# Performance work log

Hardware: AMD Instinct MI355X
Metric: run time of the kernel (lower is better)

Reference implementation:

```python
import jax, jax.numpy as jnp
import numpy as np

N_HEAD = 16


def setup_inputs() -> dict:
    key = jax.random.key(0)
    ks = jax.random.split(key, 6)
    B, T, C = 8, 1024, 1024
    s = 0.02
    return {
        "x": jax.random.normal(ks[0], (B, T, C), dtype=jnp.float32),
        "Wk": jax.random.normal(ks[1], (C, C), dtype=jnp.float32) * s,
        "bk": jnp.zeros((C,), dtype=jnp.float32),
        "Wq": jax.random.normal(ks[2], (C, C), dtype=jnp.float32) * s,
        "bq": jnp.zeros((C,), dtype=jnp.float32),
        "Wv": jax.random.normal(ks[3], (C, C), dtype=jnp.float32) * s,
        "bv": jnp.zeros((C,), dtype=jnp.float32),
        "Wp": jax.random.normal(ks[4], (C, C), dtype=jnp.float32) * s,
        "bp": jnp.zeros((C,), dtype=jnp.float32),
    }


def reference(x, Wk, bk, Wq, bq, Wv, bv, Wp, bp):
    B, T, C = x.shape
    H = N_HEAD
    d = C // H
    # QKV projections, split heads -> [B, H, T, d]
    k = (x @ Wk + bk).reshape(B, T, H, d).transpose(0, 2, 1, 3)
    q = (x @ Wq + bq).reshape(B, T, H, d).transpose(0, 2, 1, 3)
    v = (x @ Wv + bv).reshape(B, T, H, d).transpose(0, 2, 1, 3)
    # NOTE: original computes K @ Q^T (not Q @ K^T) and scales by C^-0.5
    attn = jnp.einsum('bhid,bhjd->bhij', k, q) * (C ** -0.5)
    mask = jnp.tril(jnp.ones((T, T), dtype=bool))  # tril==0 positions masked
    attn = jnp.where(mask, attn, -jnp.inf)
    attn = jax.nn.softmax(attn, axis=-1)
    out = jnp.einsum('bhij,bhjd->bhid', attn, v)  # [B, H, T, d]
    out = out.transpose(0, 2, 1, 3).reshape(B, T, C)
    return out @ Wp + bp
```

## Files before the change

### kernel.cpp

```cpp
#include <hip/hip_runtime.h>

typedef unsigned short u16;
typedef unsigned int u32;
typedef __bf16 bf16x8 __attribute__((ext_vector_type(8)));
typedef float f32x4 __attribute__((ext_vector_type(4)));

__device__ __forceinline__ u16 f2bf(float f) {
  u32 u = __builtin_bit_cast(u32, f);
  u += 0x7fffu + ((u >> 16) & 1u);
  return (u16)(u >> 16);
}

#define GLOAD_LDS16(g, l) __builtin_amdgcn_global_load_lds( \
    (const __attribute__((address_space(1))) void*)(g),     \
    (__attribute__((address_space(3))) void*)(l), 16, 0, 0)

#define SCK (0.03125f * 1.44269504088896f)

__global__ __launch_bounds__(256) void cvt_x_k(const float* __restrict__ x,
                                               u16* __restrict__ xb) {
  size_t i = (size_t)blockIdx.x * 256 + threadIdx.x;
  const float4* p = reinterpret_cast<const float4*>(x) + i * 2;
  float4 a = p[0], b = p[1];
  u32 w0 = f2bf(a.x) | ((u32)f2bf(a.y) << 16);
  u32 w1 = f2bf(a.z) | ((u32)f2bf(a.w) << 16);
  u32 w2 = f2bf(b.x) | ((u32)f2bf(b.y) << 16);
  u32 w3 = f2bf(b.z) | ((u32)f2bf(b.w) << 16);
  uint4 o; o.x = w0; o.y = w1; o.z = w2; o.w = w3;
  *reinterpret_cast<uint4*>(xb + i * 8) = o;
}

__global__ __launch_bounds__(256) void transW_k(const float* __restrict__ W0,
                                                const float* __restrict__ W1,
                                                const float* __restrict__ W2,
                                                const float* __restrict__ W3,
                                                u16* __restrict__ WT) {
  __shared__ float tile[64][65];
  const float* W = blockIdx.z == 0 ? W0 : blockIdx.z == 1 ? W1
                 : blockIdx.z == 2 ? W2 : W3;
  u16* dst = WT + (size_t)blockIdx.z * 1024 * 1024;
  const int k0 = blockIdx.x * 64, n0 = blockIdx.y * 64;
  const int tid = threadIdx.x;
  const int rr = tid >> 4, c4 = (tid & 15) * 4;
#pragma unroll
  for (int p = 0; p < 4; ++p) {
    int r = rr + p * 16;
    float4 v = *reinterpret_cast<const float4*>(W + (size_t)(k0 + r) * 1024 + n0 + c4);
    tile[r][c4 + 0] = v.x; tile[r][c4 + 1] = v.y;
    tile[r][c4 + 2] = v.z; tile[r][c4 + 3] = v.w;
  }
  __syncthreads();
#pragma unroll
  for (int p = 0; p < 4; ++p) {
    int nl = rr + p * 16;
    u32 w0 = f2bf(tile[c4 + 0][nl]) | ((u32)f2bf(tile[c4 + 1][nl]) << 16);
    u32 w1 = f2bf(tile[c4 + 2][nl]) | ((u32)f2bf(tile[c4 + 3][nl]) << 16);
    uint2 o; o.x = w0; o.y = w1;
    *reinterpret_cast<uint2*>(dst + (size_t)(n0 + nl) * 1024 + k0 + c4) = o;
  }
}

template <int MODE>
__global__ __launch_bounds__(256) void gemm_k(
    const u16* __restrict__ A, const u16* __restrict__ BT,
    const float* __restrict__ bias0, const float* __restrict__ bias1,
    const float* __restrict__ bias2,
    u16* __restrict__ out_k, u16* __restrict__ out_q, u16* __restrict__ out_vT,
    float* __restrict__ out_f) {
  __shared__ __align__(16) u16 As[128 * 32];
  __shared__ __align__(16) u16 Bs[128 * 32];
  const int tid = threadIdx.x;
  const int row0 = blockIdx.x * 128, col0 = blockIdx.y * 128;
  const int w = tid >> 6, lane = tid & 63;
  const int wr = (w >> 1) * 64, wc = (w & 1) * 64;
  const int fr = lane & 15, fq = lane >> 4, koff = fq * 8;

  const int e0 = tid * 8;
  const int srow = e0 >> 5, scol = e0 & 31;
  const u16* Ag = A + (size_t)(row0 + srow) * 1024 + scol;
  const u16* Bg = BT + (size_t)(col0 + srow) * 1024 + scol;

  f32x4 acc[4][4] = {};

  for (int kt = 0; kt < 32; ++kt) {
    const int k0 = kt * 32;
    GLOAD_LDS16(Ag + k0, &As[e0]);
    GLOAD_LDS16(Ag + k0 + 64 * 1024, &As[e0 + 2048]);
    GLOAD_LDS16(Bg + k0, &Bs[e0]);
    GLOAD_LDS16(Bg + k0 + 64 * 1024, &Bs[e0 + 2048]);
    __syncthreads();
    bf16x8 a[4], b[4];
#pragma unroll
    for (int m = 0; m < 4; ++m)
      a[m] = *reinterpret_cast<const bf16x8*>(&As[(wr + m * 16 + fr) * 32 + koff]);
#pragma unroll
    for (int n = 0; n < 4; ++n)
      b[n] = *reinterpret_cast<const bf16x8*>(&Bs[(wc + n * 16 + fr) * 32 + koff]);
#pragma unroll
    for (int m = 0; m < 4; ++m)
#pragma unroll
      for (int n = 0; n < 4; ++n)
        acc[m][n] = __builtin_amdgcn_mfma_f32_16x16x32_bf16(a[m], b[n], acc[m][n], 0, 0, 0);
    __syncthreads();
  }

  if constexpr (MODE == 0) {
    const int which = col0 >> 10;
    const float* bias = which == 0 ? bias0 : which == 1 ? bias1 : bias2;
#pragma unroll
    for (int m = 0; m < 4; ++m) {
#pragma unroll
      for (int n = 0; n < 4; ++n) {
        const int rg = row0 + wr + m * 16 + fq * 4;
        const int cg = col0 + wc + n * 16 + fr;
        const int nloc = cg & 1023;
        const float bv = bias[nloc];
        if (which == 0) {
#pragma unroll
          for (int r = 0; r < 4; ++r)
            out_k[(size_t)(rg + r) * 1024 + nloc] = f2bf((acc[m][n][r] + bv) * SCK);
        } else if (which == 1) {
#pragma unroll
          for (int r = 0; r < 4; ++r)
            out_q[(size_t)(rg + r) * 1024 + nloc] = f2bf(acc[m][n][r] + bv);
        } else {
          const int bb = rg >> 10, t = rg & 1023;
          const int h = nloc >> 6, dl = nloc & 63;
          u32 w0 = f2bf(acc[m][n][0] + bv) | ((u32)f2bf(acc[m][n][1] + bv) << 16);
          u32 w1 = f2bf(acc[m][n][2] + bv) | ((u32)f2bf(acc[m][n][3] + bv) << 16);
          uint2 ov; ov.x = w0; ov.y = w1;
          *reinterpret_cast<uint2*>(out_vT + ((size_t)(bb * 16 + h) * 64 + dl) * 1024 + t) = ov;
        }
      }
    }
  } else {
#pragma unroll
    for (int m = 0; m < 4; ++m)
#pragma unroll
      for (int n = 0; n < 4; ++n) {
        const int rg = row0 + wr + m * 16 + fq * 4;
        const int cg = col0 + wc + n * 16 + fr;
        const float bv = bias0[cg];
#pragma unroll
        for (int r = 0; r < 4; ++r)
          out_f[(size_t)(rg + r) * 1024 + cg] = acc[m][n][r] + bv;
      }
  }
}

__global__ __launch_bounds__(256, 4) void attn_k(const u16* __restrict__ Q,
                                                 const u16* __restrict__ K,
                                                 const u16* __restrict__ vT,
                                                 u16* __restrict__ O) {
  __shared__ __align__(16) u16 KsA[4096], KsB[4096], VsA[4096], VsB[4096];
  __shared__ __align__(16) u16 Plds[4][16][40];
  const int tid = threadIdx.x;
  const int w = tid >> 6, lane = tid & 63;
  const int fr = lane & 15, fq = lane >> 4, koff = fq * 8;

  const int n = blockIdx.x + 8 * (blockIdx.y + 16 * blockIdx.z);
  const int xcd = n & 7, rest = n >> 3;
  const int g = rest >> 3, pair = rest & 7;
  const int hb = xcd + 8 * g;
  const int h = hb & 15, b = hb >> 4;

  const size_t bstride = (size_t)1024 * 1024;
  const u16* Qb = Q + b * bstride + h * 64;
  const u16* Kg = K + b * bstride + h * 64;
  const u16* Vg = vT + ((size_t)(b * 16 + h) * 64) * 1024;

  const int srow = tid >> 3;
  const int scb = (tid & 7) ^ (srow & 7);
  const u16* KgT = Kg + (size_t)srow * 1024 + scb * 8;
  const u16* VgT = Vg + (size_t)srow * 1024 + scb * 8;

  const int vK0 = fr * 128 + ((fq ^ (fr & 7)) << 4);
  const int vK1 = vK0 ^ 64;
  const int pw = w * 1280 + fq * 320 + fr * 2;
  const int pr = w * 1280 + fr * 80 + fq * 16;

#define STAGE(KS, VS, jt) do {                                          \
    GLOAD_LDS16(KgT + (size_t)(jt) * 65536, &KS[tid * 8]);              \
    GLOAD_LDS16(KgT + (size_t)(jt) * 65536 + 32 * 1024, &KS[2048 + tid * 8]); \
    GLOAD_LDS16(VgT + (jt) * 64, &VS[tid * 8]);                         \
    GLOAD_LDS16(VgT + (jt) * 64 + 32 * 1024, &VS[2048 + tid * 8]);      \
  } while (0)

#pragma unroll 1
  for (int ph = 0; ph < 2; ++ph) {
    const int T = ph ? (15 - pair) : pair;
    const int i0 = T * 64;
    const int ibase = i0 + w * 16;

    bf16x8 aq0 = *reinterpret_cast<const bf16x8*>(&Qb[(size_t)(ibase + fr) * 1024 + koff]);
    bf16x8 aq1 = *reinterpret_cast<const bf16x8*>(&Qb[(size_t)(ibase + fr) * 1024 + koff + 32]);

    f32x4 o[4] = {};
    float lp[4] = {0.f, 0.f, 0.f, 0.f};

    auto compute = [&](const u16* KS, const u16* VS, bool diag) {
      const char* Kc = reinterpret_cast<const char*>(KS);
      const char* Vc = reinterpret_cast<const char*>(VS);
      f32x4 s[4];
#pragma unroll
      for (int jc = 0; jc < 4; ++jc) {
        bf16x8 bk0 = *reinterpret_cast<const bf16x8*>(Kc + vK0 + jc * 2048);
        bf16x8 bk1 = *reinterpret_cast<const bf16x8*>(Kc + vK1 + jc * 2048);
        f32x4 z = {};
        z = __builtin_amdgcn_mfma_f32_16x16x32_bf16(aq0, bk0, z, 0, 0, 0);
        s[jc] = __builtin_amdgcn_mfma_f32_16x16x32_bf16(aq1, bk1, z, 0, 0, 0);
      }
      bf16x8 bv0[4], bv1[4];
#pragma unroll
      for (int dn = 0; dn < 4; ++dn) {
        bv0[dn] = *reinterpret_cast<const bf16x8*>(Vc + vK0 + dn * 2048);
        bv1[dn] = *reinterpret_cast<const bf16x8*>(Vc + vK1 + dn * 2048);
      }
      float p[4][4];
      if (diag) {
#pragma unroll
        for (int r = 0; r < 4; ++r) {
          const int il = w * 16 + fq * 4 + r;
#pragma unroll
          for (int jc = 0; jc < 4; ++jc) {
            const int jl = jc * 16 + fr;
            p[jc][r] = (jl <= il) ? __builtin_amdgcn_exp2f(s[jc][r]) : 0.f;
          }
        }
      } else {
#pragma unroll
        for (int r = 0; r < 4; ++r)
#pragma unroll
          for (int jc = 0; jc < 4; ++jc)
            p[jc][r] = __builtin_amdgcn_exp2f(s[jc][r]);
      }
#pragma unroll
      for (int r = 0; r < 4; ++r)
        lp[r] += (p[0][r] + p[1][r]) + (p[2][r] + p[3][r]);
      char* Pc = reinterpret_cast<char*>(&Plds[0][0][0]);
#pragma unroll
      for (int jh = 0; jh < 2; ++jh) {
#pragma unroll
        for (int r = 0; r < 4; ++r)
#pragma unroll
          for (int j2 = 0; j2 < 2; ++j2)
            *reinterpret_cast<u16*>(Pc + pw + r * 80 + j2 * 32) = f2bf(p[jh * 2 + j2][r]);
        bf16x8 ap = *reinterpret_cast<const bf16x8*>(Pc + pr);
#pragma unroll
        for (int dn = 0; dn < 4; ++dn)
          o[dn] = __builtin_amdgcn_mfma_f32_16x16x32_bf16(ap, jh ? bv1[dn] : bv0[dn],
                                                          o[dn], 0, 0, 0);
      }
    };

    STAGE(KsA, VsA, 0);
    int t = 0;
    while (true) {
      {
        const bool more = t < T;
        if (more) STAGE(KsB, VsB, t + 1);
        if (more) { asm volatile("s_waitcnt vmcnt(4)" ::: "memory"); }
        else      { asm volatile("s_waitcnt vmcnt(0)" ::: "memory"); }
        __builtin_amdgcn_s_barrier();
        compute(KsA, VsA, t == T);
        __builtin_amdgcn_s_barrier();
        if (!more) break;
        ++t;
      }
      {
        const bool more = t < T;
        if (more) STAGE(KsA, VsA, t + 1);
        if (more) { asm volatile("s_waitcnt vmcnt(4)" ::: "memory"); }
        else      { asm volatile("s_waitcnt vmcnt(0)" ::: "memory"); }
        __builtin_amdgcn_s_barrier();
        compute(KsB, VsB, t == T);
        __builtin_amdgcn_s_barrier();
        if (!more) break;
        ++t;
      }
    }

#pragma unroll
    for (int x = 1; x < 16; x <<= 1)
#pragma unroll
      for (int r = 0; r < 4; ++r) lp[r] += __shfl_xor(lp[r], x);
#pragma unroll
    for (int r = 0; r < 4; ++r) {
      const float inv = 1.f / lp[r];
      const int ig = ibase + fq * 4 + r;
#pragma unroll
      for (int dn = 0; dn < 4; ++dn)
        O[((size_t)b * 1024 + ig) * 1024 + h * 64 + dn * 16 + fr] = f2bf(o[dn][r] * inv);
    }
  }
#undef STAGE
}

extern "C" void kernel_launch(void* const* d_in, const int* in_sizes, int n_in,
                              void* d_out, int out_size, void* d_ws, size_t ws_size,
                              hipStream_t stream) {
  const float* x  = (const float*)d_in[0];
  const float* Wk = (const float*)d_in[1];
  const float* bk = (const float*)d_in[2];
  const float* Wq = (const float*)d_in[3];
  const float* bq = (const float*)d_in[4];
  const float* Wv = (const float*)d_in[5];
  const float* bv = (const float*)d_in[6];
  const float* Wp = (const float*)d_in[7];
  const float* bp = (const float*)d_in[8];
  float* out = (float*)d_out;

  char* ws = (char*)d_ws;
  u16* xb   = (u16*)(ws);
  u16* WT   = (u16*)(ws + ((size_t)16 << 20));
  u16* kbuf = (u16*)(ws + ((size_t)24 << 20));
  u16* qbuf = (u16*)(ws + ((size_t)40 << 20));
  u16* vT   = (u16*)(ws + ((size_t)56 << 20));
  u16* aout = (u16*)(ws + ((size_t)72 << 20));

  cvt_x_k<<<4096, 256, 0, stream>>>(x, xb);
  transW_k<<<dim3(16, 16, 4), 256, 0, stream>>>(Wk, Wq, Wv, Wp, WT);
  gemm_k<0><<<dim3(64, 24), 256, 0, stream>>>(xb, WT, bk, bq, bv,
                                              kbuf, qbuf, vT, nullptr);
  attn_k<<<dim3(8, 16, 8), 256, 0, stream>>>(kbuf, qbuf, vT, aout);
  gemm_k<1><<<dim3(64, 8), 256, 0, stream>>>(aout, WT + (size_t)3 * 1024 * 1024,
                                             bp, nullptr, nullptr,
                                             nullptr, nullptr, nullptr, out);
}
```

Measured before the change: 153.7 us.

## Rewrite projection GEMMs as 8-wave double-buffered kernels with swizzled LDS

Replaces the 128x128, K=32 single-buffered GEMM with a 512-thread kernel using 256xBN tiles (BN 192 for QKV, 128 for output projection) and K=64 stages. The stages are double-buffered in LDS with an XOR-swizzled layout to avoid bank conflicts. MFMA work is split into four quadrants interleaved with LDS reads and the next global prefetch, using explicit waitcnt, raised wave priority and barriers. Block IDs are remapped across XCDs for cache locality. The goal is to hide global and LDS latency and raise MFMA utilisation, at the cost of heavy register pressure and fragile hand-tuned wait counts.

```diff
diff --git a/kernel.cpp b/kernel.cpp
--- a/kernel.cpp
+++ b/kernel.cpp
@@ -16,6 +16,10 @@
     (__attribute__((address_space(3))) void*)(l), 16, 0, 0)
 
 #define SCK (0.03125f * 1.44269504088896f)
+
+#define BARF() do { asm volatile("" ::: "memory"); \
+                    __builtin_amdgcn_s_barrier();  \
+                    asm volatile("" ::: "memory"); } while (0)
 
 __global__ __launch_bounds__(256) void cvt_x_k(const float* __restrict__ x,
                                                u16* __restrict__ xb) {
@@ -61,89 +65,185 @@
 }
 
 template <int MODE>
-__global__ __launch_bounds__(256) void gemm_k(
+__global__ __launch_bounds__(512, 2) void gemm8_k(
     const u16* __restrict__ A, const u16* __restrict__ BT,
     const float* __restrict__ bias0, const float* __restrict__ bias1,
     const float* __restrict__ bias2,
     u16* __restrict__ out_k, u16* __restrict__ out_q, u16* __restrict__ out_vT,
     float* __restrict__ out_f) {
-  __shared__ __align__(16) u16 As[128 * 32];
-  __shared__ __align__(16) u16 Bs[128 * 32];
+  constexpr int BN = (MODE == 0) ? 192 : 128;
+  constexpr int NB = BN / 64;
+  constexpr int NBLO = NB - NB / 2;
+  constexpr int NBHI = NB / 2;
+  constexpr int LPT = 4 + NB;
+  constexpr int WCW = BN / 4;
+
+  __shared__ __align__(16) u16 As[2][256 * 64];
+  __shared__ __align__(16) u16 Bs[2][BN * 64];
+
   const int tid = threadIdx.x;
-  const int row0 = blockIdx.x * 128, col0 = blockIdx.y * 128;
   const int w = tid >> 6, lane = tid & 63;
-  const int wr = (w >> 1) * 64, wc = (w & 1) * 64;
-  const int fr = lane & 15, fq = lane >> 4, koff = fq * 8;
-
-  const int e0 = tid * 8;
-  const int srow = e0 >> 5, scol = e0 & 31;
-  const u16* Ag = A + (size_t)(row0 + srow) * 1024 + scol;
-  const u16* Bg = BT + (size_t)(col0 + srow) * 1024 + scol;
-
-  f32x4 acc[4][4] = {};
-
-  for (int kt = 0; kt < 32; ++kt) {
-    const int k0 = kt * 32;
-    GLOAD_LDS16(Ag + k0, &As[e0]);
-    GLOAD_LDS16(Ag + k0 + 64 * 1024, &As[e0 + 2048]);
-    GLOAD_LDS16(Bg + k0, &Bs[e0]);
-    GLOAD_LDS16(Bg + k0 + 64 * 1024, &Bs[e0 + 2048]);
-    __syncthreads();
-    bf16x8 a[4], b[4];
-#pragma unroll
-    for (int m = 0; m < 4; ++m)
-      a[m] = *reinterpret_cast<const bf16x8*>(&As[(wr + m * 16 + fr) * 32 + koff]);
-#pragma unroll
-    for (int n = 0; n < 4; ++n)
-      b[n] = *reinterpret_cast<const bf16x8*>(&Bs[(wc + n * 16 + fr) * 32 + koff]);
-#pragma unroll
-    for (int m = 0; m < 4; ++m)
-#pragma unroll
-      for (int n = 0; n < 4; ++n)
-        acc[m][n] = __builtin_amdgcn_mfma_f32_16x16x32_bf16(a[m], b[n], acc[m][n], 0, 0, 0);
-    __syncthreads();
+  const int wr = w >> 2, wc = w & 3;
+  const int fr = lane & 15, fq = lane >> 4;
+  const int d = fr & 7;
+
+  const int cpx = (int)gridDim.x >> 3;
+  const int bid = (int)blockIdx.x;
+  const int swz = (bid & 7) * cpx + (bid >> 3);
+  const int bx = swz & 31;
+  const int by = swz >> 5;
+  const int row0 = bx * 256, col0 = by * BN;
+
+  const int r0 = tid >> 3;
+  const int cbg = (tid & 7) ^ (r0 & 7);
+  const u16* Asrc = A + (size_t)(row0 + r0) * 1024 + cbg * 8;
+  const u16* Bsrc = BT + (size_t)(col0 + r0) * 1024 + cbg * 8;
+
+#define STAGE8(buf, t) do {                                                  \
+    _Pragma("unroll")                                                        \
+    for (int sw = 0; sw < 4; ++sw)                                           \
+      GLOAD_LDS16(Asrc + (size_t)sw * 65536 + (t) * 64,                      \
+                  &As[buf][sw * 4096 + tid * 8]);                            \
+    _Pragma("unroll")                                                        \
+    for (int sw = 0; sw < NB; ++sw)                                          \
+      GLOAD_LDS16(Bsrc + (size_t)sw * 65536 + (t) * 64,                      \
+                  &Bs[buf][sw * 4096 + tid * 8]);                            \
+  } while (0)
+
+#define AOFF(mb, kk) ((wr * 128 + (mb) * 16 + fr) * 128 + (((((kk) << 2) | fq) ^ d) << 4))
+#define BOFF(nb, kk) ((wc * WCW + (nb) * 16 + fr) * 128 + (((((kk) << 2) | fq) ^ d) << 4))
+
+  f32x4 acc[8][NB] = {};
+
+  STAGE8(0, 0);
+  STAGE8(1, 1);
+  asm volatile("s_waitcnt vmcnt(%0)" :: "n"(LPT) : "memory");
+  BARF();
+
+#pragma unroll 1
+  for (int g = 0; g < 16; ++g) {
+    const int buf = g & 1;
+    const char* Ac = (const char*)&As[buf][0];
+    const char* Bc = (const char*)&Bs[buf][0];
+    bf16x8 a03[4][2], a47[4][2], blo[NBLO][2], bhi[NBHI][2];
+
+#pragma unroll
+    for (int mb = 0; mb < 4; ++mb)
+#pragma unroll
+      for (int kk = 0; kk < 2; ++kk)
+        a03[mb][kk] = *(const bf16x8*)(Ac + AOFF(mb, kk));
+#pragma unroll
+    for (int nb = 0; nb < NBLO; ++nb)
+#pragma unroll
+      for (int kk = 0; kk < 2; ++kk)
+        blo[nb][kk] = *(const bf16x8*)(Bc + BOFF(nb, kk));
+#pragma unroll
+    for (int nb = 0; nb < NBHI; ++nb)
+#pragma unroll
+      for (int kk = 0; kk < 2; ++kk)
+        bhi[nb][kk] = *(const bf16x8*)(Bc + BOFF(NBLO + nb, kk));
+    asm volatile("s_waitcnt lgkmcnt(%0)" :: "n"(2 * NBHI) : "memory");
+    __builtin_amdgcn_s_setprio(1);
+#pragma unroll
+    for (int mb = 0; mb < 4; ++mb)
+#pragma unroll
+      for (int nb = 0; nb < NBLO; ++nb)
+#pragma unroll
+        for (int kk = 0; kk < 2; ++kk)
+          acc[mb][nb] = __builtin_amdgcn_mfma_f32_16x16x32_bf16(
+              a03[mb][kk], blo[nb][kk], acc[mb][nb], 0, 0, 0);
+    __builtin_amdgcn_s_setprio(0);
+    BARF();
+
+#pragma unroll
+    for (int mb = 0; mb < 4; ++mb)
+#pragma unroll
+      for (int kk = 0; kk < 2; ++kk)
+        a47[mb][kk] = *(const bf16x8*)(Ac + AOFF(4 + mb, kk));
+    asm volatile("s_waitcnt lgkmcnt(8)" ::: "memory");
+    __builtin_amdgcn_s_setprio(1);
+#pragma unroll
+    for (int mb = 0; mb < 4; ++mb)
+#pragma unroll
+      for (int nb = 0; nb < NBHI; ++nb)
+#pragma unroll
+        for (int kk = 0; kk < 2; ++kk)
+          acc[mb][NBLO + nb] = __builtin_amdgcn_mfma_f32_16x16x32_bf16(
+              a03[mb][kk], bhi[nb][kk], acc[mb][NBLO + nb], 0, 0, 0);
+    __builtin_amdgcn_s_setprio(0);
+    BARF();
+
+    asm volatile("s_waitcnt lgkmcnt(0)" ::: "memory");
+    __builtin_amdgcn_s_setprio(1);
+#pragma unroll
+    for (int mb = 0; mb < 4; ++mb)
+#pragma unroll
+      for (int nb = 0; nb < NBHI; ++nb)
+#pragma unroll
+        for (int kk = 0; kk < 2; ++kk)
+          acc[4 + mb][NBLO + nb] = __builtin_amdgcn_mfma_f32_16x16x32_bf16(
+              a47[mb][kk], bhi[nb][kk], acc[4 + mb][NBLO + nb], 0, 0, 0);
+    __builtin_amdgcn_s_setprio(0);
+    BARF();
+
+    if (g + 2 < 16) STAGE8(buf, g + 2);
+    __builtin_amdgcn_s_setprio(1);
+#pragma unroll
+    for (int mb = 0; mb < 4; ++mb)
+#pragma unroll
+      for (int nb = 0; nb < NBLO; ++nb)
+#pragma unroll
+        for (int kk = 0; kk < 2; ++kk)
+          acc[4 + mb][nb] = __builtin_amdgcn_mfma_f32_16x16x32_bf16(
+              a47[mb][kk], blo[nb][kk], acc[4 + mb][nb], 0, 0, 0);
+    __builtin_amdgcn_s_setprio(0);
+    if (g <= 13)      asm volatile("s_waitcnt vmcnt(%0)" :: "n"(LPT) : "memory");
+    else if (g == 14) asm volatile("s_waitcnt vmcnt(0)" ::: "memory");
+    BARF();
   }
+#undef STAGE8
+#undef AOFF
+#undef BOFF
 
   if constexpr (MODE == 0) {
-    const int which = col0 >> 10;
-    const float* bias = which == 0 ? bias0 : which == 1 ? bias1 : bias2;
-#pragma unroll
-    for (int m = 0; m < 4; ++m) {
-#pragma unroll
-      for (int n = 0; n < 4; ++n) {
-        const int rg = row0 + wr + m * 16 + fq * 4;
-        const int cg = col0 + wc + n * 16 + fr;
+#pragma unroll
+    for (int mb = 0; mb < 8; ++mb) {
+#pragma unroll
+      for (int nb = 0; nb < NB; ++nb) {
+        const int rg = row0 + wr * 128 + mb * 16 + fq * 4;
+        const int cg = col0 + wc * WCW + nb * 16 + fr;
+        const int which = cg >> 10;
         const int nloc = cg & 1023;
-        const float bv = bias[nloc];
+        const float bv = (which == 0 ? bias0 : which == 1 ? bias1 : bias2)[nloc];
         if (which == 0) {
 #pragma unroll
           for (int r = 0; r < 4; ++r)
-            out_k[(size_t)(rg + r) * 1024 + nloc] = f2bf((acc[m][n][r] + bv) * SCK);
+            out_k[(size_t)(rg + r) * 1024 + nloc] = f2bf((acc[mb][nb][r] + bv) * SCK);
         } else if (which == 1) {
 #pragma unroll
           for (int r = 0; r < 4; ++r)
-            out_q[(size_t)(rg + r) * 1024 + nloc] = f2bf(acc[m][n][r] + bv);
+            out_q[(size_t)(rg + r) * 1024 + nloc] = f2bf(acc[mb][nb][r] + bv);
         } else {
           const int bb = rg >> 10, t = rg & 1023;
-          const int h = nloc >> 6, dl = nloc & 63;
-          u32 w0 = f2bf(acc[m][n][0] + bv) | ((u32)f2bf(acc[m][n][1] + bv) << 16);
-          u32 w1 = f2bf(acc[m][n][2] + bv) | ((u32)f2bf(acc[m][n][3] + bv) << 16);
+          const int hh = nloc >> 6, dl = nloc & 63;
+          u32 w0 = f2bf(acc[mb][nb][0] + bv) | ((u32)f2bf(acc[mb][nb][1] + bv) << 16);
+          u32 w1 = f2bf(acc[mb][nb][2] + bv) | ((u32)f2bf(acc[mb][nb][3] + bv) << 16);
           uint2 ov; ov.x = w0; ov.y = w1;
-          *reinterpret_cast<uint2*>(out_vT + ((size_t)(bb * 16 + h) * 64 + dl) * 1024 + t) = ov;
+          *reinterpret_cast<uint2*>(out_vT + ((size_t)(bb * 16 + hh) * 64 + dl) * 1024 + t) = ov;
         }
       }
     }
   } else {
 #pragma unroll
-    for (int m = 0; m < 4; ++m)
-#pragma unroll
-      for (int n = 0; n < 4; ++n) {
-        const int rg = row0 + wr + m * 16 + fq * 4;
-        const int cg = col0 + wc + n * 16 + fr;
+    for (int mb = 0; mb < 8; ++mb)
+#pragma unroll
+      for (int nb = 0; nb < NB; ++nb) {
+        const int rg = row0 + wr * 128 + mb * 16 + fq * 4;
+        const int cg = col0 + wc * WCW + nb * 16 + fr;
         const float bv = bias0[cg];
 #pragma unroll
         for (int r = 0; r < 4; ++r)
-          out_f[(size_t)(rg + r) * 1024 + cg] = acc[m][n][r] + bv;
+          out_f[(size_t)(rg + r) * 1024 + cg] = acc[mb][nb][r] + bv;
       }
   }
 }
@@ -320,10 +420,10 @@
 
   cvt_x_k<<<4096, 256, 0, stream>>>(x, xb);
   transW_k<<<dim3(16, 16, 4), 256, 0, stream>>>(Wk, Wq, Wv, Wp, WT);
-  gemm_k<0><<<dim3(64, 24), 256, 0, stream>>>(xb, WT, bk, bq, bv,
-                                              kbuf, qbuf, vT, nullptr);
+  gemm8_k<0><<<512, 512, 0, stream>>>(xb, WT, bk, bq, bv,
+                                      kbuf, qbuf, vT, nullptr);
   attn_k<<<dim3(8, 16, 8), 256, 0, stream>>>(kbuf, qbuf, vT, aout);
-  gemm_k<1><<<dim3(64, 8), 256, 0, stream>>>(aout, WT + (size_t)3 * 1024 * 1024,
-                                             bp, nullptr, nullptr,
-                                             nullptr, nullptr, nullptr, out);
-}
+  gemm8_k<1><<<256, 512, 0, stream>>>(aout, WT + (size_t)3 * 1024 * 1024,
+                                      bp, nullptr, nullptr,
+                                      nullptr, nullptr, nullptr, out);
+}
```

Measured after the change: 153.8 us. About the same (+0.1%).

## Double-buffer GEMM LDS tiles with async prefetch, swizzle, and XCD-aware block mapping

Applied to the files above, without the earlier changes.

Rewrites the projection GEMM main loop to double-buffer the A/B tiles in LDS. The next-but-one K slice is issued via global_load_lds right after the fragment reads, so global loads overlap the MFMA work, and the full __syncthreads pair is replaced by explicit waitcnt plus a raw barrier. It also XOR-swizzles the 16-byte chunks in LDS to avoid bank conflicts and remaps a 1D grid so neighbouring row tiles land on the same XCD for L2 reuse. It raises MFMA priority with setprio and requests occupancy 4. LDS use doubles, and the hand-placed waitcnt counts must exactly match the outstanding loads.

```diff
diff --git a/kernel.cpp b/kernel.cpp
--- a/kernel.cpp
+++ b/kernel.cpp
@@ -16,6 +16,10 @@
     (__attribute__((address_space(3))) void*)(l), 16, 0, 0)
 
 #define SCK (0.03125f * 1.44269504088896f)
+
+#define BARF() do { asm volatile("" ::: "memory"); \
+                    __builtin_amdgcn_s_barrier();  \
+                    asm volatile("" ::: "memory"); } while (0)
 
 __global__ __launch_bounds__(256) void cvt_x_k(const float* __restrict__ x,
                                                u16* __restrict__ xb) {
@@ -61,89 +65,121 @@
 }
 
 template <int MODE>
-__global__ __launch_bounds__(256) void gemm_k(
+__global__ __launch_bounds__(256, 4) void gemm4_k(
     const u16* __restrict__ A, const u16* __restrict__ BT,
     const float* __restrict__ bias0, const float* __restrict__ bias1,
     const float* __restrict__ bias2,
     u16* __restrict__ out_k, u16* __restrict__ out_q, u16* __restrict__ out_vT,
     float* __restrict__ out_f) {
-  __shared__ __align__(16) u16 As[128 * 32];
-  __shared__ __align__(16) u16 Bs[128 * 32];
+  __shared__ __align__(16) u16 As[2][4096];
+  __shared__ __align__(16) u16 Bs[2][4096];
+
   const int tid = threadIdx.x;
-  const int row0 = blockIdx.x * 128, col0 = blockIdx.y * 128;
   const int w = tid >> 6, lane = tid & 63;
-  const int wr = (w >> 1) * 64, wc = (w & 1) * 64;
-  const int fr = lane & 15, fq = lane >> 4, koff = fq * 8;
-
-  const int e0 = tid * 8;
-  const int srow = e0 >> 5, scol = e0 & 31;
-  const u16* Ag = A + (size_t)(row0 + srow) * 1024 + scol;
-  const u16* Bg = BT + (size_t)(col0 + srow) * 1024 + scol;
+  const int wr = w >> 1, wc = w & 1;
+  const int fr = lane & 15, fq = lane >> 4;
+
+  const int bid = (int)blockIdx.x;
+  const int xcd = bid & 7, c = bid >> 3;
+  const int bx = xcd * 8 + (c & 7);
+  const int by = c >> 3;
+  const int row0 = bx * 128, col0 = by * 128;
+
+  const int srow = tid >> 2;
+  const int scb = (tid & 3) ^ ((srow >> 1) & 3);
+  const u16* Asrc = A + (size_t)(row0 + srow) * 1024 + scb * 8;
+  const u16* Bsrc = BT + (size_t)(col0 + srow) * 1024 + scb * 8;
+
+#define STAGE4(buf, t) do {                                        \
+    GLOAD_LDS16(Asrc + (t) * 32,         &As[buf][tid * 8]);       \
+    GLOAD_LDS16(Asrc + (t) * 32 + 65536, &As[buf][2048 + tid * 8]);\
+    GLOAD_LDS16(Bsrc + (t) * 32,         &Bs[buf][tid * 8]);       \
+    GLOAD_LDS16(Bsrc + (t) * 32 + 65536, &Bs[buf][2048 + tid * 8]);\
+  } while (0)
+
+  const int chs = (fq ^ ((fr >> 1) & 3)) << 4;
+#define AOFF(mb) ((wr * 64 + (mb) * 16 + fr) * 64 + chs)
+#define BOFF(nb) ((wc * 64 + (nb) * 16 + fr) * 64 + chs)
 
   f32x4 acc[4][4] = {};
 
-  for (int kt = 0; kt < 32; ++kt) {
-    const int k0 = kt * 32;
-    GLOAD_LDS16(Ag + k0, &As[e0]);
-    GLOAD_LDS16(Ag + k0 + 64 * 1024, &As[e0 + 2048]);
-    GLOAD_LDS16(Bg + k0, &Bs[e0]);
-    GLOAD_LDS16(Bg + k0 + 64 * 1024, &Bs[e0 + 2048]);
-    __syncthreads();
+  STAGE4(0, 0);
+  STAGE4(1, 1);
+  asm volatile("s_waitcnt vmcnt(4)" ::: "memory");
+  BARF();
+
+#pragma unroll 1
+  for (int g = 0; g < 32; ++g) {
+    const int buf = g & 1;
+    const char* Ac = (const char*)&As[buf][0];
+    const char* Bc = (const char*)&Bs[buf][0];
     bf16x8 a[4], b[4];
 #pragma unroll
-    for (int m = 0; m < 4; ++m)
-      a[m] = *reinterpret_cast<const bf16x8*>(&As[(wr + m * 16 + fr) * 32 + koff]);
-#pragma unroll
-    for (int n = 0; n < 4; ++n)
-      b[n] = *reinterpret_cast<const bf16x8*>(&Bs[(wc + n * 16 + fr) * 32 + koff]);
-#pragma unroll
-    for (int m = 0; m < 4; ++m)
-#pragma unroll
-      for (int n = 0; n < 4; ++n)
-        acc[m][n] = __builtin_amdgcn_mfma_f32_16x16x32_bf16(a[m], b[n], acc[m][n], 0, 0, 0);
-    __syncthreads();
-  }
+    for (int mb = 0; mb < 4; ++mb) a[mb] = *(const bf16x8*)(Ac + AOFF(mb));
+#pragma unroll
+    for (int nb = 0; nb < 4; ++nb) b[nb] = *(const bf16x8*)(Bc + BOFF(nb));
+    asm volatile("s_waitcnt lgkmcnt(0)" ::: "memory");
+    BARF();
+    if (g + 2 < 32) STAGE4(buf, g + 2);
+    __builtin_amdgcn_s_setprio(1);
+#pragma unroll
+    for (int mb = 0; mb < 4; ++mb)
+#pragma unroll
+      for (int nb = 0; nb < 4; ++nb)
+        acc[mb][nb] = __builtin_amdgcn_mfma_f32_16x16x32_bf16(a[mb], b[nb],
+                                                              acc[mb][nb], 0, 0, 0);
+    __builtin_amdgcn_s_setprio(0);
+    if (g < 30) {
+      asm volatile("s_waitcnt vmcnt(4)" ::: "memory");
+      BARF();
+    } else if (g == 30) {
+      asm volatile("s_waitcnt vmcnt(0)" ::: "memory");
+      BARF();
+    }
+  }
+#undef STAGE4
+#undef AOFF
+#undef BOFF
 
   if constexpr (MODE == 0) {
-    const int which = col0 >> 10;
-    const float* bias = which == 0 ? bias0 : which == 1 ? bias1 : bias2;
-#pragma unroll
-    for (int m = 0; m < 4; ++m) {
-#pragma unroll
-      for (int n = 0; n < 4; ++n) {
-        const int rg = row0 + wr + m * 16 + fq * 4;
-        const int cg = col0 + wc + n * 16 + fr;
+#pragma unroll
+    for (int mb = 0; mb < 4; ++mb) {
+#pragma unroll
+      for (int nb = 0; nb < 4; ++nb) {
+        const int rg = row0 + wr * 64 + mb * 16 + fq * 4;
+        const int cg = col0 + wc * 64 + nb * 16 + fr;
+        const int which = cg >> 10;
         const int nloc = cg & 1023;
-        const float bv = bias[nloc];
+        const float bv = (which == 0 ? bias0 : which == 1 ? bias1 : bias2)[nloc];
         if (which == 0) {
 #pragma unroll
           for (int r = 0; r < 4; ++r)
-            out_k[(size_t)(rg + r) * 1024 + nloc] = f2bf((acc[m][n][r] + bv) * SCK);
+            out_k[(size_t)(rg + r) * 1024 + nloc] = f2bf((acc[mb][nb][r] + bv) * SCK);
         } else if (which == 1) {
 #pragma unroll
           for (int r = 0; r < 4; ++r)
-            out_q[(size_t)(rg + r) * 1024 + nloc] = f2bf(acc[m][n][r] + bv);
+            out_q[(size_t)(rg + r) * 1024 + nloc] = f2bf(acc[mb][nb][r] + bv);
         } else {
           const int bb = rg >> 10, t = rg & 1023;
-          const int h = nloc >> 6, dl = nloc & 63;
-          u32 w0 = f2bf(acc[m][n][0] + bv) | ((u32)f2bf(acc[m][n][1] + bv) << 16);
-          u32 w1 = f2bf(acc[m][n][2] + bv) | ((u32)f2bf(acc[m][n][3] + bv) << 16);
+          const int hh = nloc >> 6, dl = nloc & 63;
+          u32 w0 = f2bf(acc[mb][nb][0] + bv) | ((u32)f2bf(acc[mb][nb][1] + bv) << 16);
+          u32 w1 = f2bf(acc[mb][nb][2] + bv) | ((u32)f2bf(acc[mb][nb][3] + bv) << 16);
           uint2 ov; ov.x = w0; ov.y = w1;
-          *reinterpret_cast<uint2*>(out_vT + ((size_t)(bb * 16 + h) * 64 + dl) * 1024 + t) = ov;
+          *reinterpret_cast<uint2*>(out_vT + ((size_t)(bb * 16 + hh) * 64 + dl) * 1024 + t) = ov;
         }
       }
     }
   } else {
 #pragma unroll
-    for (int m = 0; m < 4; ++m)
-#pragma unroll
-      for (int n = 0; n < 4; ++n) {
-        const int rg = row0 + wr + m * 16 + fq * 4;
-        const int cg = col0 + wc + n * 16 + fr;
+    for (int mb = 0; mb < 4; ++mb)
+#pragma unroll
+      for (int nb = 0; nb < 4; ++nb) {
+        const int rg = row0 + wr * 64 + mb * 16 + fq * 4;
+        const int cg = col0 + wc * 64 + nb * 16 + fr;
         const float bv = bias0[cg];
 #pragma unroll
         for (int r = 0; r < 4; ++r)
-          out_f[(size_t)(rg + r) * 1024 + cg] = acc[m][n][r] + bv;
+          out_f[(size_t)(rg + r) * 1024 + cg] = acc[mb][nb][r] + bv;
       }
   }
 }
@@ -320,10 +356,10 @@
 
   cvt_x_k<<<4096, 256, 0, stream>>>(x, xb);
   transW_k<<<dim3(16, 16, 4), 256, 0, stream>>>(Wk, Wq, Wv, Wp, WT);
-  gemm_k<0><<<dim3(64, 24), 256, 0, stream>>>(xb, WT, bk, bq, bv,
-                                              kbuf, qbuf, vT, nullptr);
+  gemm4_k<0><<<1536, 256, 0, stream>>>(xb, WT, bk, bq, bv,
+                                       kbuf, qbuf, vT, nullptr);
   attn_k<<<dim3(8, 16, 8), 256, 0, stream>>>(kbuf, qbuf, vT, aout);
-  gemm_k<1><<<dim3(64, 8), 256, 0, stream>>>(aout, WT + (size_t)3 * 1024 * 1024,
-                                             bp, nullptr, nullptr,
-                                             nullptr, nullptr, nullptr, out);
-}
+  gemm4_k<1><<<512, 256, 0, stream>>>(aout, WT + (size_t)3 * 1024 * 1024,
+                                      bp, nullptr, nullptr,
+                                      nullptr, nullptr, nullptr, out);
+}
```

Measured after the change: 143.3 us. 1.07x faster.
